# Optimization experiments

Hardware: AMD Instinct MI355X
Metric: run time of the kernel (lower is better)

Reference implementation:

```python
import jax, jax.numpy as jnp
import numpy as np

N = 8192        # total nodes in the batch of graphs
E = 262144      # edges (avg degree 32)
F_IN = 128      # input node features
G = 64          # graphs in batch
C = 10          # classes
K1, K2, K3 = 4096, 2048, 1024  # int(0.5*N), int(0.5*K1), int(0.5*K2)


def setup_inputs() -> dict:
    key = jax.random.key(0)
    ks = jax.random.split(key, 16)
    def lin(k, i, o):
        return jax.random.normal(k, (i, o), jnp.float32) / np.float32(np.sqrt(i))
    return {
        "x": jax.random.normal(ks[0], (N, F_IN), jnp.float32),
        "edge_index": jax.random.randint(ks[1], (2, E), 0, N),
        "batch": jnp.sort(jax.random.randint(ks[2], (N,), 0, G)),
        "W1": lin(ks[3], F_IN, 32), "b1": jnp.zeros((32,), jnp.float32),
        "W2": lin(ks[4], 32, 64),   "b2": jnp.zeros((64,), jnp.float32),
        "W3": lin(ks[5], 64, 128),  "b3": jnp.zeros((128,), jnp.float32),
        "W4": lin(ks[6], 128, 256), "b4": jnp.zeros((256,), jnp.float32),
        "W5": lin(ks[7], 384, 128), "b5": jnp.zeros((128,), jnp.float32),
        "W6": lin(ks[8], 192, 64),  "b6": jnp.zeros((64,), jnp.float32),
        "W7": lin(ks[9], 96, 32),   "b7": jnp.zeros((32,), jnp.float32),
        "p1": jax.random.normal(ks[10], (32,), jnp.float32),
        "p2": jax.random.normal(ks[11], (64,), jnp.float32),
        "p3": jax.random.normal(ks[12], (128,), jnp.float32),
        "Wl1": lin(ks[13], 64, 64),
        "Wc": lin(ks[14], 64, C), "bc": jnp.zeros((C,), jnp.float32),
    }


def _gcn(A, x, W, b):
    # PyG GCNConv (improved=False): out = D^-1/2 (A+I) D^-1/2 propagated src->dst.
    n = A.shape[0]
    Ah = A + jnp.eye(n, dtype=A.dtype)
    deg = Ah.sum(axis=0)                                  # degree at targets (cols)
    dinv = jnp.where(deg > 0, deg ** -0.5, 0.0).astype(A.dtype)
    An = dinv[:, None] * Ah * dinv[None, :]               # edge norm d[src]^-.5 * d[dst]^-.5
    return An.T @ (x @ W) + b                             # out[dst] += norm * (xW)[src]


def _gpool(A, x, p, k):
    # GPool: scores = Linear(x)/||p||, top-k select, gate by sigmoid, reindex dense adj.
    scores = (x @ p) / jnp.linalg.norm(p)                 # [n]
    vals, idx = jax.lax.top_k(scores, k)
    xp = x[idx] * jax.nn.sigmoid(vals)[:, None]
    Ap = (A[idx][:, idx] > 0).astype(x.dtype)             # dense_to_sparse rebinarizes
    return xp, Ap, idx


def reference(x, edge_index, batch, W1, b1, W2, b2, W3, b3, W4, b4, W5, b5,
              W6, b6, W7, b7, p1, p2, p3, Wl1, Wc, bc):
    elu = jax.nn.elu
    # to_dense_adj: dense N x N adjacency (duplicate edges accumulate)
    A = jnp.zeros((N, N), x.dtype).at[edge_index[0], edge_index[1]].add(1.0)
    x1 = elu(_gcn(A, x, W1, b1))
    x2, A2, i2 = _gpool(A, x1, p1, K1); x2 = elu(x2)
    x3 = elu(_gcn(A2, x2, W2, b2))
    x4, A4, i4 = _gpool(A2, x3, p2, K2); x4 = elu(x4)
    x5 = elu(_gcn(A4, x4, W3, b3))
    x6, A6, i6 = _gpool(A4, x5, p3, K3); x6 = elu(x6)
    x7 = elu(_gcn(A6, x6, W4, b4))
    u = jnp.zeros((K2, x7.shape[1]), x7.dtype).at[i6].set(x7)   # GUnpool
    x8 = elu(jnp.concatenate([u, x5], axis=1))
    x9 = elu(_gcn(A4, x8, W5, b5))
    u = jnp.zeros((K1, x9.shape[1]), x9.dtype).at[i4].set(x9)
    x10 = elu(jnp.concatenate([u, x3], axis=1))
    x11 = elu(_gcn(A2, x10, W6, b6))
    u = jnp.zeros((N, x11.shape[1]), x11.dtype).at[i2].set(x11)
    x12 = elu(jnp.concatenate([u, x1], axis=1))
    x13 = elu(_gcn(A, x12, W7, b7))
    gmax = jax.ops.segment_max(x13, batch, num_segments=G)      # global max pool
    gsum = jax.ops.segment_sum(x13, batch, num_segments=G)
    cnt = jax.ops.segment_sum(jnp.ones((N, 1), x13.dtype), batch, num_segments=G)
    h = elu(jnp.concatenate([gmax, gsum / cnt], axis=1))        # [G, 64]
    h = elu(h @ Wl1)
    return jax.nn.log_softmax(h @ Wc + bc, axis=-1)
```

## Files before the change

### kernel.cpp

```cpp
#include <hip/hip_runtime.h>
#include <math.h>

#define NN 8192
#define EE 262144
#define GG 64
#define CC 10
#define KK1 4096
#define KK2 2048
#define KK3 1024
#define PITCH 128

typedef unsigned long long ull;

__device__ __forceinline__ float eluf(float x) { return x > 0.f ? x : expm1f(x); }
__device__ __forceinline__ float sigf(float x) { return 1.f / (1.f + expf(-x)); }
__device__ __forceinline__ unsigned f2s(float f) {
    unsigned u = __float_as_uint(f);
    return (u & 0x80000000u) ? ~u : (u | 0x80000000u);
}

__global__ void k_init(const int* __restrict__ ei, int* __restrict__ cnt1,
                       int* __restrict__ csr1, const int* __restrict__ batch,
                       int* __restrict__ gstart, const float* __restrict__ X,
                       const float* __restrict__ W, float* __restrict__ Y) {
    __shared__ float Xs[32][33];
    __shared__ float Ws[32][36];
    int tid = threadIdx.x;
    if ((int)blockIdx.x >= 1024) {
        int txn = tid & 7, tym = tid >> 3;
        int m0 = ((int)blockIdx.x - 1024) * 32;
        float4 acc = make_float4(0.f, 0.f, 0.f, 0.f);
        for (int k0 = 0; k0 < 128; k0 += 32) {
            int r = tid >> 3, c4 = (tid & 7) << 2;
            *(float4*)&Xs[r][c4] = *(const float4*)&X[(size_t)(m0 + r) * 128 + k0 + c4];
            *(float4*)&Ws[r][c4] = *(const float4*)&W[(size_t)(k0 + r) * 32 + c4];
            __syncthreads();
#pragma unroll 8
            for (int kk = 0; kk < 32; kk++) {
                float4 wv = *(const float4*)&Ws[kk][txn * 4];
                float xv = Xs[tym][kk];
                acc.x += xv * wv.x; acc.y += xv * wv.y;
                acc.z += xv * wv.z; acc.w += xv * wv.w;
            }
            __syncthreads();
        }
        *(float4*)&Y[(size_t)(m0 + tym) * 32 + txn * 4] = acc;
        return;
    }
    int e = blockIdx.x * 256 + tid;
    int s = ei[e], d = ei[EE + e];
    int pos = atomicAdd(&cnt1[d], 1);
    csr1[(d << 7) + pos] = s;
    if (e < NN) {
        int g = batch[e];
        int prev = (e == 0) ? -1 : batch[e - 1];
        for (int gg = prev + 1; gg <= g; gg++) gstart[gg] = e;
        if (e == NN - 1)
            for (int gg = g + 1; gg <= GG; gg++) gstart[gg] = NN;
    }
}

template<int L1>
__global__ void k_pool_sub(const float* __restrict__ x, const float* __restrict__ score,
                           const int* __restrict__ idx, int k, int F,
                           float* __restrict__ xout, int nPool,
                           const int* __restrict__ csrP, const int* __restrict__ roffP,
                           const int* __restrict__ degP,
                           const int* __restrict__ invmap,
                           int* __restrict__ csrO, int* __restrict__ roffO,
                           int* __restrict__ degO, float* __restrict__ dinvO) {
    if ((int)blockIdx.x < nPool) {
        int t = blockIdx.x * 256 + threadIdx.x;
        if (t >= k * F) return;
        int r = t / F, f = t - r * F;
        int j = idx[r];
        xout[t] = eluf(x[(size_t)j * F + f] * sigf(score[j]));
        return;
    }
    int wid = (((int)blockIdx.x - nPool) * 256 + (int)threadIdx.x) >> 6;
    int lane = threadIdx.x & 63;
    if (wid >= k) return;
    int j = idx[wid];
    int cnt = 0;
    if (L1) {
        int j0 = j << 7;
        int len = degP[j];
        int e0 = (lane < len) ? csrP[j0 + lane] : -1;
        int e1 = (64 + lane < len) ? csrP[j0 + 64 + lane] : -1;
        bool dup0 = false, dup1 = false;
        for (int q = 0; q < len - 1; q++) {
            int vq = (q < 64) ? __shfl(e0, q, 64) : __shfl(e1, q - 64, 64);
            if (lane > q && e0 == vq) dup0 = true;
            if (64 + lane > q && e1 == vq) dup1 = true;
        }
        {
            bool sel = (lane < len) && !dup0;
            int val = 0;
            if (sel) { int v = invmap[e0]; if (v > 0) val = v - 1; else sel = false; }
            ull m = __ballot(sel);
            if (sel) { int off = __popcll(m & ((1ull << lane) - 1ull)); csrO[j0 + cnt + off] = val; }
            cnt += __popcll(m);
        }
        {
            bool sel = (64 + lane < len) && !dup1;
            int val = 0;
            if (sel) { int v = invmap[e1]; if (v > 0) val = v - 1; else sel = false; }
            ull m = __ballot(sel);
            if (sel) { int off = __popcll(m & ((1ull << lane) - 1ull)); csrO[j0 + cnt + off] = val; }
            cnt += __popcll(m);
        }
        if (lane == 0) {
            roffO[wid] = j0;
            degO[wid] = cnt;
            dinvO[wid] = 1.f / sqrtf((float)(cnt + 1));
        }
    } else {
        int j0 = roffP[j];
        int len = degP[j];
        for (int base = 0; base < len; base += 64) {
            bool sel = false;
            int val = 0;
            if (base + lane < len) {
                int e = csrP[j0 + base + lane];
                int v = invmap[e];
                if (v > 0) { sel = true; val = v - 1; }
            }
            ull m = __ballot(sel);
            if (sel) { int off = __popcll(m & ((1ull << lane) - 1ull)); csrO[j0 + cnt + off] = val; }
            cnt += __popcll(m);
        }
        if (lane == 0) {
            roffO[wid] = j0;
            degO[wid] = cnt;
            dinvO[wid] = 1.f / sqrtf((float)(cnt + 1));
        }
    }
}

__global__ void k_gemm(const float* __restrict__ X, const float* __restrict__ W,
                       float* __restrict__ Y, int M, int K, int F) {
    __shared__ float Xs[32][33];
    __shared__ float Ws[32][36];
    int tid = threadIdx.x;
    int txn = tid & 7, tym = tid >> 3;
    int m0 = blockIdx.x * 32, n0 = blockIdx.y * 32;
    float4 acc = make_float4(0.f, 0.f, 0.f, 0.f);
    for (int k0 = 0; k0 < K; k0 += 32) {
        {
            int r = tid >> 3, c4 = (tid & 7) << 2;
            *(float4*)&Xs[r][c4] = *(const float4*)&X[(size_t)(m0 + r) * K + k0 + c4];
            *(float4*)&Ws[r][c4] = *(const float4*)&W[(size_t)(k0 + r) * F + n0 + c4];
        }
        __syncthreads();
#pragma unroll 8
        for (int kk = 0; kk < 32; kk++) {
            float4 wv = *(const float4*)&Ws[kk][txn * 4];
            float xv = Xs[tym][kk];
            acc.x += xv * wv.x; acc.y += xv * wv.y;
            acc.z += xv * wv.z; acc.w += xv * wv.w;
        }
        __syncthreads();
    }
    *(float4*)&Y[(size_t)(m0 + tym) * F + n0 + txn * 4] = acc;
}

__global__ void k_gemm_up(const float* __restrict__ xl, const int* __restrict__ inv,
                          const float* __restrict__ xr, int Fl, int Fr,
                          const float* __restrict__ W, float* __restrict__ Y,
                          int M, int K, int F) {
    __shared__ float Xs[32][33];
    __shared__ float Ws[32][36];
    __shared__ int sIdx[32];
    int tid = threadIdx.x;
    int txn = tid & 7, tym = tid >> 3;
    int m0 = blockIdx.x * 32, n0 = blockIdx.y * 32;
    if (tid < 32) sIdx[tid] = inv[m0 + tid];
    float4 acc = make_float4(0.f, 0.f, 0.f, 0.f);
    __syncthreads();
    for (int k0 = 0; k0 < K; k0 += 32) {
        {
            int r = tid >> 3, c4 = (tid & 7) << 2;
            int kk = k0 + c4;
            float4 v;
            if (kk < Fl) {
                int rr = sIdx[r];
                v = (rr > 0) ? *(const float4*)&xl[(size_t)(rr - 1) * Fl + kk]
                             : make_float4(0.f, 0.f, 0.f, 0.f);
            } else {
                v = *(const float4*)&xr[(size_t)(m0 + r) * Fr + (kk - Fl)];
            }
            v.x = eluf(v.x); v.y = eluf(v.y); v.z = eluf(v.z); v.w = eluf(v.w);
            *(float4*)&Xs[r][c4] = v;
            *(float4*)&Ws[r][c4] = *(const float4*)&W[(size_t)(k0 + r) * F + n0 + c4];
        }
        __syncthreads();
#pragma unroll 8
        for (int kk = 0; kk < 32; kk++) {
            float4 wv = *(const float4*)&Ws[kk][txn * 4];
            float xv = Xs[tym][kk];
            acc.x += xv * wv.x; acc.y += xv * wv.y;
            acc.z += xv * wv.z; acc.w += xv * wv.w;
        }
        __syncthreads();
    }
    *(float4*)&Y[(size_t)(m0 + tym) * F + n0 + txn * 4] = acc;
}

template<int LOGF, int SCORE, int L1, int LS>
__global__ void k_prop(const int* __restrict__ csr, const int* __restrict__ roff,
                       const int* __restrict__ deg, const float* __restrict__ dinv,
                       const float* __restrict__ xW, const float* __restrict__ b,
                       float* __restrict__ xout, const float* __restrict__ p,
                       float* __restrict__ score) {
    constexpr int FQ = 1 << (LOGF - 2);
    constexpr int S = 1 << LS;
    constexpr int RL = FQ * S;
    const float4* xW4 = (const float4*)xW;
    int t = blockIdx.x * 256 + threadIdx.x;
    int d = t >> (LOGF - 2 + LS);
    int rem = t & (RL - 1);
    int q = rem >> LS, h = rem & (S - 1);
    int j0 = L1 ? (d << 7) : roff[d];
    int dg = deg[d];
    int j1 = j0 + dg;
    float dd = L1 ? (1.f / sqrtf((float)(dg + 1))) : dinv[d];
    int idx = (d << (LOGF - 2)) + q;
    float4 sum;
    if (h == 0) {
        float4 v0 = xW4[idx];
        sum = make_float4(dd * v0.x, dd * v0.y, dd * v0.z, dd * v0.w);
    } else {
        sum = make_float4(0.f, 0.f, 0.f, 0.f);
    }
    for (int j = j0 + h; j < j1; j += S) {
        int s = csr[j];
        float ds = L1 ? (1.f / sqrtf((float)(deg[s] + 1))) : dinv[s];
        float4 xv = xW4[(s << (LOGF - 2)) + q];
        sum.x += ds * xv.x; sum.y += ds * xv.y;
        sum.z += ds * xv.z; sum.w += ds * xv.w;
    }
#pragma unroll
    for (int m = 1; m < S; m <<= 1) {
        sum.x += __shfl_xor(sum.x, m, 64);
        sum.y += __shfl_xor(sum.y, m, 64);
        sum.z += __shfl_xor(sum.z, m, 64);
        sum.w += __shfl_xor(sum.w, m, 64);
    }
    float4 bv = *(const float4*)&b[q << 2];
    float4 o;
    o.x = eluf(dd * sum.x + bv.x);
    o.y = eluf(dd * sum.y + bv.y);
    o.z = eluf(dd * sum.z + bv.z);
    o.w = eluf(dd * sum.w + bv.w);
    if (h == 0) ((float4*)xout)[idx] = o;
    if (SCORE) {
        float4 pv = *(const float4*)&p[q << 2];
        float sc = 0.f, nr = 0.f;
        if (h == 0) {
            sc = o.x * pv.x + o.y * pv.y + o.z * pv.z + o.w * pv.w;
            nr = pv.x * pv.x + pv.y * pv.y + pv.z * pv.z + pv.w * pv.w;
        }
#pragma unroll
        for (int m = RL >> 1; m >= 1; m >>= 1) {
            sc += __shfl_xor(sc, m, 64);
            nr += __shfl_xor(nr, m, 64);
        }
        if (rem == 0) score[d] = sc / sqrtf(nr);
    }
}

__device__ __forceinline__ ull cex_shfl(ull v, int st, bool takeMax) {
    ull pv = __shfl_xor(v, st, 64);
    return takeMax ? (v > pv ? v : pv) : (v < pv ? v : pv);
}
__device__ __forceinline__ void cexr(ull& a, ull& b, bool desc) {
    if (desc ? (a < b) : (a > b)) { ull x = a; a = b; b = x; }
}

__global__ void k_wsort(const float* __restrict__ score, ull* __restrict__ keys,
                        int last, int k, int* __restrict__ out_idx,
                        int* __restrict__ invmap) {
    __shared__ ull sk[2048];
    int tid = threadIdx.x;
    int base = blockIdx.x << 11;
    int giA = base + tid, giB = giA + 1024;
    ull a = ((ull)f2s(score[giA]) << 32) | (unsigned)(~giA);
    ull b = ((ull)f2s(score[giB]) << 32) | (unsigned)(~giB);
    for (int sz = 2; sz <= 2048; sz <<= 1) {
        int st = sz >> 1;
        if (st >= 64) {
            sk[tid] = a; sk[tid + 1024] = b;
            __syncthreads();
            for (; st >= 64; st >>= 1) {
                int i = ((tid & ~(st - 1)) << 1) | (tid & (st - 1));
                int j = i | st;
                ull u = sk[i], v = sk[j];
                bool desc = (((base + i) & sz) == 0);
                if (desc ? (u < v) : (u > v)) { sk[i] = v; sk[j] = u; }
                __syncthreads();
            }
            a = sk[tid]; b = sk[tid + 1024];
        }
        for (; st >= 1; st >>= 1) {
            bool low = (tid & st) == 0;
            bool descA = ((giA & sz) == 0);
            bool descB = ((giB & sz) == 0);
            a = cex_shfl(a, st, descA == low);
            b = cex_shfl(b, st, descB == low);
        }
    }
    if (last) {
        if (giA < k) {
            int j = (int)(~(unsigned)(a & 0xFFFFFFFFu));
            out_idx[giA] = j; invmap[j] = giA + 1;
        }
        if (giB < k) {
            int j = (int)(~(unsigned)(b & 0xFFFFFFFFu));
            out_idx[giB] = j; invmap[j] = giB + 1;
        }
    } else {
        keys[giA] = a; keys[giB] = b;
    }
}

__global__ void k_sort4k(const float* __restrict__ score, ull* __restrict__ keys,
                         int last, int k, int* __restrict__ out_idx,
                         int* __restrict__ invmap) {
    __shared__ ull sk[4096];
    int tid = threadIdx.x;
    int base = blockIdx.x << 12;
    int p0 = base + tid, p1 = p0 + 1024, p2 = p0 + 2048, p3 = p0 + 3072;
    ull k0 = ((ull)f2s(score[p0]) << 32) | (unsigned)(~p0);
    ull k1 = ((ull)f2s(score[p1]) << 32) | (unsigned)(~p1);
    ull k2 = ((ull)f2s(score[p2]) << 32) | (unsigned)(~p2);
    ull k3 = ((ull)f2s(score[p3]) << 32) | (unsigned)(~p3);
    for (int sz = 2; sz <= 4096; sz <<= 1) {
        int st = sz >> 1;
        if (st >= 64) {
            sk[tid] = k0; sk[tid + 1024] = k1; sk[tid + 2048] = k2; sk[tid + 3072] = k3;
            __syncthreads();
            for (; st >= 64; st >>= 1) {
                for (int pp = tid; pp < 2048; pp += 1024) {
                    int i = ((pp & ~(st - 1)) << 1) | (pp & (st - 1));
                    int jj = i | st;
                    ull u = sk[i], v = sk[jj];
                    bool desc = (((base + i) & sz) == 0);
                    if (desc ? (u < v) : (u > v)) { sk[i] = v; sk[jj] = u; }
                }
                __syncthreads();
            }
            k0 = sk[tid]; k1 = sk[tid + 1024]; k2 = sk[tid + 2048]; k3 = sk[tid + 3072];
        }
        for (; st >= 1; st >>= 1) {
            bool low = (tid & st) == 0;
            k0 = cex_shfl(k0, st, ((p0 & sz) == 0) == low);
            k1 = cex_shfl(k1, st, ((p1 & sz) == 0) == low);
            k2 = cex_shfl(k2, st, ((p2 & sz) == 0) == low);
            k3 = cex_shfl(k3, st, ((p3 & sz) == 0) == low);
        }
    }
    if (last) {
        int j;
        if (p0 < k) { j = (int)(~(unsigned)(k0 & 0xFFFFFFFFu)); out_idx[p0] = j; invmap[j] = p0 + 1; }
        if (p1 < k) { j = (int)(~(unsigned)(k1 & 0xFFFFFFFFu)); out_idx[p1] = j; invmap[j] = p1 + 1; }
        if (p2 < k) { j = (int)(~(unsigned)(k2 & 0xFFFFFFFFu)); out_idx[p2] = j; invmap[j] = p2 + 1; }
        if (p3 < k) { j = (int)(~(unsigned)(k3 & 0xFFFFFFFFu)); out_idx[p3] = j; invmap[j] = p3 + 1; }
    } else {
        keys[p0] = k0; keys[p1] = k1; keys[p2] = k2; keys[p3] = k3;
    }
}

__global__ void k_stage8k_f(const ull* __restrict__ keys, int* __restrict__ out_idx,
                            int* __restrict__ invmap) {
    __shared__ ull sk[4096];
    int tid = threadIdx.x;
    ull a0 = keys[tid],        a1 = keys[tid + 1024];
    ull a2 = keys[tid + 2048], a3 = keys[tid + 3072];
    ull b0 = keys[tid + 4096], b1 = keys[tid + 5120];
    ull b2 = keys[tid + 6144], b3 = keys[tid + 7168];
    cexr(a0, b0, true); cexr(a1, b1, true);
    cexr(a2, b2, true); cexr(a3, b3, true);
    cexr(a0, a2, true); cexr(a1, a3, true);
    sk[tid] = a0; sk[tid + 1024] = a1; sk[tid + 2048] = a2; sk[tid + 3072] = a3;
    __syncthreads();
    for (int st = 1024; st >= 64; st >>= 1) {
        for (int pp = tid; pp < 2048; pp += 1024) {
            int i = ((pp & ~(st - 1)) << 1) | (pp & (st - 1));
            int j = i | st;
            ull u = sk[i], v = sk[j];
            if (u < v) { sk[i] = v; sk[j] = u; }
        }
        __syncthreads();
    }
    a0 = sk[tid]; a1 = sk[tid + 1024]; a2 = sk[tid + 2048]; a3 = sk[tid + 3072];
    for (int st = 32; st >= 1; st >>= 1) {
        bool low = (tid & st) == 0;
        a0 = cex_shfl(a0, st, low);
        a1 = cex_shfl(a1, st, low);
        a2 = cex_shfl(a2, st, low);
        a3 = cex_shfl(a3, st, low);
    }
    int p, j;
    p = tid;        j = (int)(~(unsigned)(a0 & 0xFFFFFFFFu)); out_idx[p] = j; invmap[j] = p + 1;
    p = tid + 1024; j = (int)(~(unsigned)(a1 & 0xFFFFFFFFu)); out_idx[p] = j; invmap[j] = p + 1;
    p = tid + 2048; j = (int)(~(unsigned)(a2 & 0xFFFFFFFFu)); out_idx[p] = j; invmap[j] = p + 1;
    p = tid + 3072; j = (int)(~(unsigned)(a3 & 0xFFFFFFFFu)); out_idx[p] = j; invmap[j] = p + 1;
}

__global__ void k_finale(const float* __restrict__ x13, const int* __restrict__ gstart,
                         const float* __restrict__ Wl1, const float* __restrict__ Wc,
                         const float* __restrict__ bc, float* __restrict__ out) {
    __shared__ float sm[8][32], ss[8][32];
    __shared__ float h0[64], h1[64], lg[CC];
    int g = blockIdx.x;
    int j0 = gstart[g], j1 = gstart[g + 1];
    int t = threadIdx.x;
    int f = t & 31, r = t >> 5;
    float m = -INFINITY, s = 0.f;
    for (int j = j0 + r; j < j1; j += 8) {
        float v = x13[(j << 5) + f];
        m = fmaxf(m, v);
        s += v;
    }
    sm[r][f] = m; ss[r][f] = s;
    __syncthreads();
    if (t < 32) {
        float mm = sm[0][t], sss = ss[0][t];
        for (int i = 1; i < 8; i++) { mm = fmaxf(mm, sm[i][t]); sss += ss[i][t]; }
        h0[t] = eluf(mm);
        h0[32 + t] = eluf(sss / (float)(j1 - j0));
    }
    __syncthreads();
    if (t < 64) {
        float sum = 0.f;
        for (int kk = 0; kk < 64; kk++) sum += h0[kk] * Wl1[kk * 64 + t];
        h1[t] = eluf(sum);
    }
    __syncthreads();
    if (t < CC) {
        float sum = bc[t];
        for (int kk = 0; kk < 64; kk++) sum += h1[kk] * Wc[kk * CC + t];
        lg[t] = sum;
    }
    __syncthreads();
    if (t == 0) {
        float mm = -1e30f;
        for (int c = 0; c < CC; c++) mm = fmaxf(mm, lg[c]);
        float se = 0.f;
        for (int c = 0; c < CC; c++) se += expf(lg[c] - mm);
        float lse = mm + logf(se);
        for (int c = 0; c < CC; c++) out[g * CC + c] = lg[c] - lse;
    }
}

static void run_topk(const float* score, ull* keys, int n, int k, int* out_idx,
                     int* invmap, hipStream_t stream) {
    if (n == 2048) {
        k_wsort<<<1, 1024, 0, stream>>>(score, keys, 1, k, out_idx, invmap);
    } else if (n == 4096) {
        k_sort4k<<<1, 1024, 0, stream>>>(score, keys, 1, k, out_idx, invmap);
    } else {
        k_sort4k<<<2, 1024, 0, stream>>>(score, keys, 0, k, out_idx, invmap);
        k_stage8k_f<<<1, 1024, 0, stream>>>(keys, out_idx, invmap);
    }
}

extern "C" void kernel_launch(void* const* d_in, const int* in_sizes, int n_in,
                              void* d_out, int out_size, void* d_ws, size_t ws_size,
                              hipStream_t stream) {
    const float* x = (const float*)d_in[0];
    const int* ei = (const int*)d_in[1];
    const int* batch = (const int*)d_in[2];
    const float* W1 = (const float*)d_in[3];  const float* b1 = (const float*)d_in[4];
    const float* W2 = (const float*)d_in[5];  const float* b2 = (const float*)d_in[6];
    const float* W3 = (const float*)d_in[7];  const float* b3 = (const float*)d_in[8];
    const float* W4 = (const float*)d_in[9];  const float* b4 = (const float*)d_in[10];
    const float* W5 = (const float*)d_in[11]; const float* b5 = (const float*)d_in[12];
    const float* W6 = (const float*)d_in[13]; const float* b6 = (const float*)d_in[14];
    const float* W7 = (const float*)d_in[15]; const float* b7 = (const float*)d_in[16];
    const float* p1 = (const float*)d_in[17];
    const float* p2 = (const float*)d_in[18];
    const float* p3 = (const float*)d_in[19];
    const float* Wl1 = (const float*)d_in[20];
    const float* Wc = (const float*)d_in[21];
    const float* bc = (const float*)d_in[22];
    float* out = (float*)d_out;
    (void)in_sizes; (void)n_in; (void)out_size; (void)ws_size;

    char* w = (char*)d_ws;
    size_t off = 0;
    auto alloc = [&](size_t bytes) -> char* {
        char* p = w + off;
        off = (off + bytes + 255) & ~(size_t)255;
        return p;
    };

    size_t zero_begin = off;
    int* cnt1 = (int*)alloc(NN * 4);
    int* pos2 = (int*)alloc(NN * 4);
    int* inv4 = (int*)alloc(KK1 * 4);
    int* inv6 = (int*)alloc(KK2 * 4);
    size_t zero_len = off - zero_begin;

    float* dinv2 = (float*)alloc(KK1 * 4);
    float* dinv3 = (float*)alloc(KK2 * 4);
    float* dinv4 = (float*)alloc(KK3 * 4);
    int* roff2 = (int*)alloc(KK1 * 4); int* deg2 = (int*)alloc(KK1 * 4);
    int* roff3 = (int*)alloc(KK2 * 4); int* deg3 = (int*)alloc(KK2 * 4);
    int* roff4 = (int*)alloc(KK3 * 4); int* deg4 = (int*)alloc(KK3 * 4);
    int* csr1 = (int*)alloc((size_t)NN * PITCH * 4);
    int* csr2 = (int*)alloc((size_t)NN * PITCH * 4);
    int* csr3 = (int*)alloc((size_t)NN * PITCH * 4);
    int* csr4 = (int*)alloc((size_t)NN * PITCH * 4);
    float* xW = (float*)alloc((size_t)262144 * 4);
    float* x1 = (float*)alloc((size_t)NN * 32 * 4);
    float* x2 = (float*)alloc((size_t)KK1 * 32 * 4);
    float* x3 = (float*)alloc((size_t)KK1 * 64 * 4);
    float* x4 = (float*)alloc((size_t)KK2 * 64 * 4);
    float* x5 = (float*)alloc((size_t)KK2 * 128 * 4);
    float* x6 = (float*)alloc((size_t)KK3 * 128 * 4);
    float* x7 = (float*)alloc((size_t)KK3 * 256 * 4);
    float* x9 = (float*)alloc((size_t)KK2 * 128 * 4);
    float* x11 = (float*)alloc((size_t)KK1 * 64 * 4);
    float* x13 = (float*)alloc((size_t)NN * 32 * 4);
    float* score1 = (float*)alloc(NN * 4);
    float* score2 = (float*)alloc(KK1 * 4);
    float* score3 = (float*)alloc(KK2 * 4);
    int* i2 = (int*)alloc(KK1 * 4);
    int* i4 = (int*)alloc(KK2 * 4);
    int* i6 = (int*)alloc(KK3 * 4);
    ull* keys = (ull*)alloc((size_t)NN * 8);
    int* gstart = (int*)alloc((GG + 1) * 4);

    hipMemsetAsync(w + zero_begin, 0, zero_len, stream);

    const int B = 256;
    k_init<<<1280, B, 0, stream>>>(ei, cnt1, csr1, batch, gstart, x, W1, xW);

    k_prop<5, 1, 1, 3><<<2048, B, 0, stream>>>(csr1, nullptr, cnt1, nullptr, xW, b1,
                                               x1, p1, score1);

    run_topk(score1, keys, NN, KK1, i2, pos2, stream);
    k_pool_sub<1><<<512 + KK1 / 4, B, 0, stream>>>(x1, score1, i2, KK1, 32, x2, 512,
                                                   csr1, nullptr, cnt1, pos2,
                                                   csr2, roff2, deg2, dinv2);

    k_gemm<<<dim3(KK1 / 32, 2), B, 0, stream>>>(x2, W2, xW, KK1, 32, 64);
    k_prop<6, 1, 0, 2><<<1024, B, 0, stream>>>(csr2, roff2, deg2, dinv2, xW, b2,
                                               x3, p2, score2);

    run_topk(score2, keys, KK1, KK2, i4, inv4, stream);
    k_pool_sub<0><<<512 + KK2 / 4, B, 0, stream>>>(x3, score2, i4, KK2, 64, x4, 512,
                                                   csr2, roff2, deg2, inv4,
                                                   csr3, roff3, deg3, dinv3);

    k_gemm<<<dim3(KK2 / 32, 4), B, 0, stream>>>(x4, W3, xW, KK2, 64, 128);
    k_prop<7, 1, 0, 1><<<512, B, 0, stream>>>(csr3, roff3, deg3, dinv3, xW, b3,
                                              x5, p3, score3);

    run_topk(score3, keys, KK2, KK3, i6, inv6, stream);
    k_pool_sub<0><<<512 + KK3 / 4, B, 0, stream>>>(x5, score3, i6, KK3, 128, x6, 512,
                                                   csr3, roff3, deg3, inv6,
                                                   csr4, roff4, deg4, dinv4);

    k_gemm<<<dim3(KK3 / 32, 8), B, 0, stream>>>(x6, W4, xW, KK3, 128, 256);
    k_prop<8, 0, 0, 1><<<512, B, 0, stream>>>(csr4, roff4, deg4, dinv4, xW, b4,
                                              x7, nullptr, nullptr);

    k_gemm_up<<<dim3(KK2 / 32, 4), B, 0, stream>>>(x7, inv6, x5, 256, 128,
                                                   W5, xW, KK2, 384, 128);
    k_prop<7, 0, 0, 2><<<1024, B, 0, stream>>>(csr3, roff3, deg3, dinv3, xW, b5,
                                               x9, nullptr, nullptr);

    k_gemm_up<<<dim3(KK1 / 32, 2), B, 0, stream>>>(x9, inv4, x3, 128, 64,
                                                   W6, xW, KK1, 192, 64);
    k_prop<6, 0, 0, 2><<<1024, B, 0, stream>>>(csr2, roff2, deg2, dinv2, xW, b6,
                                               x11, nullptr, nullptr);

    k_gemm_up<<<dim3(NN / 32, 1), B, 0, stream>>>(x11, pos2, x1, 64, 32,
                                                  W7, xW, NN, 96, 32);
    k_prop<5, 0, 1, 3><<<2048, B, 0, stream>>>(csr1, nullptr, cnt1, nullptr, xW, b7,
                                               x13, nullptr, nullptr);

    k_finale<<<GG, B, 0, stream>>>(x13, gstart, Wl1, Wc, bc, out);
}
```

Before: 341.6 us.

## Split top-k bitonic sorts into multi-block 2k sorts plus merge stages

Replaces the single-block 4096-element bitonic sort with k_wsort running on multiple blocks (each sorting 2048 keys), followed by new merge kernels (k_stage4k_f for n=4096, k_stage4k_m plus k_stage8k_f for n=8192). This spreads the early sort stages over more workgroups instead of serialising them in one or two blocks. In exchange it adds kernel launches and global-memory round trips of the key arrays between stages.

```diff
diff --git a/kernel.cpp b/kernel.cpp
--- a/kernel.cpp
+++ b/kernel.cpp
@@ -323,51 +323,35 @@
     }
 }
 
-__global__ void k_sort4k(const float* __restrict__ score, ull* __restrict__ keys,
-                         int last, int k, int* __restrict__ out_idx,
-                         int* __restrict__ invmap) {
+__global__ void k_stage4k_m(ull* __restrict__ keys) {
     __shared__ ull sk[4096];
     int tid = threadIdx.x;
     int base = blockIdx.x << 12;
-    int p0 = base + tid, p1 = p0 + 1024, p2 = p0 + 2048, p3 = p0 + 3072;
-    ull k0 = ((ull)f2s(score[p0]) << 32) | (unsigned)(~p0);
-    ull k1 = ((ull)f2s(score[p1]) << 32) | (unsigned)(~p1);
-    ull k2 = ((ull)f2s(score[p2]) << 32) | (unsigned)(~p2);
-    ull k3 = ((ull)f2s(score[p3]) << 32) | (unsigned)(~p3);
-    for (int sz = 2; sz <= 4096; sz <<= 1) {
-        int st = sz >> 1;
-        if (st >= 64) {
-            sk[tid] = k0; sk[tid + 1024] = k1; sk[tid + 2048] = k2; sk[tid + 3072] = k3;
-            __syncthreads();
-            for (; st >= 64; st >>= 1) {
-                for (int pp = tid; pp < 2048; pp += 1024) {
-                    int i = ((pp & ~(st - 1)) << 1) | (pp & (st - 1));
-                    int jj = i | st;
-                    ull u = sk[i], v = sk[jj];
-                    bool desc = (((base + i) & sz) == 0);
-                    if (desc ? (u < v) : (u > v)) { sk[i] = v; sk[jj] = u; }
-                }
-                __syncthreads();
-            }
-            k0 = sk[tid]; k1 = sk[tid + 1024]; k2 = sk[tid + 2048]; k3 = sk[tid + 3072];
-        }
-        for (; st >= 1; st >>= 1) {
-            bool low = (tid & st) == 0;
-            k0 = cex_shfl(k0, st, ((p0 & sz) == 0) == low);
-            k1 = cex_shfl(k1, st, ((p1 & sz) == 0) == low);
-            k2 = cex_shfl(k2, st, ((p2 & sz) == 0) == low);
-            k3 = cex_shfl(k3, st, ((p3 & sz) == 0) == low);
-        }
-    }
-    if (last) {
-        int j;
-        if (p0 < k) { j = (int)(~(unsigned)(k0 & 0xFFFFFFFFu)); out_idx[p0] = j; invmap[j] = p0 + 1; }
-        if (p1 < k) { j = (int)(~(unsigned)(k1 & 0xFFFFFFFFu)); out_idx[p1] = j; invmap[j] = p1 + 1; }
-        if (p2 < k) { j = (int)(~(unsigned)(k2 & 0xFFFFFFFFu)); out_idx[p2] = j; invmap[j] = p2 + 1; }
-        if (p3 < k) { j = (int)(~(unsigned)(k3 & 0xFFFFFFFFu)); out_idx[p3] = j; invmap[j] = p3 + 1; }
-    } else {
-        keys[p0] = k0; keys[p1] = k1; keys[p2] = k2; keys[p3] = k3;
-    }
+    bool desc = ((base & 4096) == 0);
+    ull k0 = keys[base + tid], k1 = keys[base + tid + 1024];
+    ull k2 = keys[base + tid + 2048], k3 = keys[base + tid + 3072];
+    cexr(k0, k2, desc); cexr(k1, k3, desc);
+    sk[tid] = k0; sk[tid + 1024] = k1; sk[tid + 2048] = k2; sk[tid + 3072] = k3;
+    __syncthreads();
+    for (int st = 1024; st >= 64; st >>= 1) {
+        for (int pp = tid; pp < 2048; pp += 1024) {
+            int i = ((pp & ~(st - 1)) << 1) | (pp & (st - 1));
+            int j = i | st;
+            ull u = sk[i], v = sk[j];
+            if (desc ? (u < v) : (u > v)) { sk[i] = v; sk[j] = u; }
+        }
+        __syncthreads();
+    }
+    k0 = sk[tid]; k1 = sk[tid + 1024]; k2 = sk[tid + 2048]; k3 = sk[tid + 3072];
+    for (int st = 32; st >= 1; st >>= 1) {
+        bool low = (tid & st) == 0;
+        k0 = cex_shfl(k0, st, desc == low);
+        k1 = cex_shfl(k1, st, desc == low);
+        k2 = cex_shfl(k2, st, desc == low);
+        k3 = cex_shfl(k3, st, desc == low);
+    }
+    keys[base + tid] = k0; keys[base + tid + 1024] = k1;
+    keys[base + tid + 2048] = k2; keys[base + tid + 3072] = k3;
 }
 
 __global__ void k_stage8k_f(const ull* __restrict__ keys, int* __restrict__ out_idx,
@@ -405,6 +389,33 @@
     p = tid + 1024; j = (int)(~(unsigned)(a1 & 0xFFFFFFFFu)); out_idx[p] = j; invmap[j] = p + 1;
     p = tid + 2048; j = (int)(~(unsigned)(a2 & 0xFFFFFFFFu)); out_idx[p] = j; invmap[j] = p + 1;
     p = tid + 3072; j = (int)(~(unsigned)(a3 & 0xFFFFFFFFu)); out_idx[p] = j; invmap[j] = p + 1;
+}
+
+__global__ void k_stage4k_f(const ull* __restrict__ keys, int* __restrict__ out_idx,
+                            int* __restrict__ invmap) {
+    __shared__ ull sk[2048];
+    int tid = threadIdx.x;
+    ull a0 = keys[tid],        a1 = keys[tid + 1024];
+    ull a2 = keys[tid + 2048], a3 = keys[tid + 3072];
+    cexr(a0, a2, true); cexr(a1, a3, true);
+    sk[tid] = a0; sk[tid + 1024] = a1;
+    __syncthreads();
+    for (int st = 1024; st >= 64; st >>= 1) {
+        int i = ((tid & ~(st - 1)) << 1) | (tid & (st - 1));
+        int j = i | st;
+        ull u = sk[i], v = sk[j];
+        if (u < v) { sk[i] = v; sk[j] = u; }
+        __syncthreads();
+    }
+    a0 = sk[tid]; a1 = sk[tid + 1024];
+    for (int st = 32; st >= 1; st >>= 1) {
+        bool low = (tid & st) == 0;
+        a0 = cex_shfl(a0, st, low);
+        a1 = cex_shfl(a1, st, low);
+    }
+    int p, j;
+    p = tid;        j = (int)(~(unsigned)(a0 & 0xFFFFFFFFu)); out_idx[p] = j; invmap[j] = p + 1;
+    p = tid + 1024; j = (int)(~(unsigned)(a1 & 0xFFFFFFFFu)); out_idx[p] = j; invmap[j] = p + 1;
 }
 
 __global__ void k_finale(const float* __restrict__ x13, const int* __restrict__ gstart,
@@ -458,9 +469,11 @@
     if (n == 2048) {
         k_wsort<<<1, 1024, 0, stream>>>(score, keys, 1, k, out_idx, invmap);
     } else if (n == 4096) {
-        k_sort4k<<<1, 1024, 0, stream>>>(score, keys, 1, k, out_idx, invmap);
+        k_wsort<<<2, 1024, 0, stream>>>(score, keys, 0, k, out_idx, invmap);
+        k_stage4k_f<<<1, 1024, 0, stream>>>(keys, out_idx, invmap);
     } else {
-        k_sort4k<<<2, 1024, 0, stream>>>(score, keys, 0, k, out_idx, invmap);
+        k_wsort<<<4, 1024, 0, stream>>>(score, keys, 0, k, out_idx, invmap);
+        k_stage4k_m<<<2, 1024, 0, stream>>>(keys);
         k_stage8k_f<<<1, 1024, 0, stream>>>(keys, out_idx, invmap);
     }
 }
```

Measured after the change: 317.5 us. 7.1% less time.
